# Kernel optimization log

Hardware: AMD Instinct MI355X
Metric: run time of the kernel (lower is better)

The kernel has to match this reference:

```python
import jax, jax.numpy as jnp
import numpy as np

B, S, D, H = 4, 2048, 1024, 16
HD = D // H
DFF = 4 * D
NUM_LAYERS = 12
RES = 1.0 / float(np.sqrt(NUM_LAYERS))
SCALE = 1.0 / float(np.sqrt(D))  # module divides by sqrt(embed_dim), not head_dim
EPS = 1e-5


def setup_inputs() -> dict:
    key = jax.random.key(0)
    ks = jax.random.split(key, 12)
    s = 0.02
    p = lambda k, shp: (jax.random.normal(k, shp, jnp.float32) * s)
    return {
        "x": jax.random.normal(ks[0], (B, S, D), jnp.float32),
        "Wq": p(ks[1], (D, D)), "bq": jnp.zeros((D,), jnp.float32),
        "Wk": p(ks[2], (D, D)), "bk": jnp.zeros((D,), jnp.float32),
        "Wv": p(ks[3], (D, D)), "bv": jnp.zeros((D,), jnp.float32),
        "Wo": p(ks[4], (D, D)), "bo": jnp.zeros((D,), jnp.float32),
        "g1": jnp.ones((D,), jnp.float32), "be1": jnp.zeros((D,), jnp.float32),
        "g2": jnp.ones((D,), jnp.float32), "be2": jnp.zeros((D,), jnp.float32),
        "W1": p(ks[5], (D, DFF)), "b1": jnp.zeros((DFF,), jnp.float32),
        "W2": p(ks[6], (DFF, D)), "b2": jnp.zeros((D,), jnp.float32),
    }


def _layernorm(x, g, b):
    m = jnp.mean(x, axis=-1, keepdims=True)
    v = jnp.mean((x - m) ** 2, axis=-1, keepdims=True)
    return (x - m) * jax.lax.rsqrt(v + EPS) * g + b


def _attention(x, Wq, bq, Wk, bk, Wv, bv, Wo, bo):
    b, s, d = x.shape
    q = (x @ Wq + bq).reshape(b, s, H, HD)
    k = (x @ Wk + bk).reshape(b, s, H, HD)
    v = (x @ Wv + bv).reshape(b, s, H, HD)
    scores = jnp.einsum('bqhd,bkhd->bhqk', q, k) * SCALE  # [B,H,S,S]
    mask = jnp.tril(jnp.ones((s, s), dtype=bool))
    scores = jnp.where(mask, scores, -jnp.inf)
    attn = jax.nn.softmax(scores, axis=-1)  # dropout_rate=0 -> identity
    out = jnp.einsum('bhqk,bkhd->bqhd', attn, v).reshape(b, s, d)
    return out @ Wo + bo


def reference(x, Wq, bq, Wk, bk, Wv, bv, Wo, bo, g1, be1, g2, be2, W1, b1, W2, b2):
    x = x + RES * _attention(_layernorm(x, g1, be1), Wq, bq, Wk, bk, Wv, bv, Wo, bo)
    h = _layernorm(x, g2, be2)
    ffn = jax.nn.relu(h @ W1 + b1) @ W2 + b2
    x = x + RES * ffn
    return x
```

## Files before the change

kernel.cpp:

```cpp
#include <hip/hip_runtime.h>

typedef unsigned short ushort_t;
typedef unsigned int uint32;
typedef __attribute__((ext_vector_type(4))) float f32x4;
typedef __attribute__((ext_vector_type(8))) short bf16x8;

#define B_   4
#define S_   2048
#define D_   1024
#define H_   16
#define HD_  64
#define DFF_ 4096
#define M_   (B_ * S_)

#define RES_   0.28867513459481287f
#define SCALE_ 0.03125f
#define EPS_   1e-5f
#define LOG2E_ 1.4426950408889634f

__device__ __forceinline__ ushort_t f2bf(float f) {
    union { float f; uint32 u; } c; c.f = f;
    uint32 u = c.u + 0x7fffu + ((c.u >> 16) & 1u);
    return (ushort_t)(u >> 16);
}
__device__ __forceinline__ float bf2f(ushort_t h) {
    union { uint32 u; float f; } c; c.u = ((uint32)h) << 16;
    return c.f;
}
__device__ __forceinline__ float fexp2(float x) {
    float r; asm("v_exp_f32 %0, %1" : "=v"(r) : "v"(x)); return r;
}
__device__ __forceinline__ uint32 cvt_pk_bf16(float lo, float hi) {
    uint32 r;
    asm("v_cvt_pk_bf16_f32 %0, %1, %2" : "=v"(r) : "v"(lo), "v"(hi));
    return r;
}

__global__ __launch_bounds__(256) void transpose_cast_kernel(
    const float* __restrict__ W, ushort_t* __restrict__ Wt, int K, int N)
{
    __shared__ float tile[32][33];
    const int bx = blockIdx.x * 32;
    const int by = blockIdx.y * 32;
    const int tx = threadIdx.x;
    const int ty = threadIdx.y;
    #pragma unroll
    for (int i = 0; i < 32; i += 8)
        tile[ty + i][tx] = W[(size_t)(by + ty + i) * N + bx + tx];
    __syncthreads();
    #pragma unroll
    for (int i = 0; i < 32; i += 8)
        Wt[(size_t)(bx + ty + i) * K + by + tx] = f2bf(tile[tx][ty + i]);
}

__global__ void concat_bias_kernel(const float* __restrict__ bq,
                                   const float* __restrict__ bk,
                                   const float* __restrict__ bv,
                                   float* __restrict__ bqkv)
{
    int i = blockIdx.x * blockDim.x + threadIdx.x;
    if (i < 3 * D_) {
        float v = (i < D_) ? bq[i] : (i < 2 * D_) ? bk[i - D_] : bv[i - 2 * D_];
        bqkv[i] = v;
    }
}

__global__ __launch_bounds__(256) void ln_kernel(
    const float* __restrict__ x, const float* __restrict__ g,
    const float* __restrict__ be, ushort_t* __restrict__ out)
{
    const int row = blockIdx.x;
    const int t = threadIdx.x;
    const int lane = t & 63;
    const int wave = t >> 6;
    const float4* xr = (const float4*)(x + (size_t)row * D_);
    float4 v = xr[t];
    float s  = v.x + v.y + v.z + v.w;
    float s2 = v.x * v.x + v.y * v.y + v.z * v.z + v.w * v.w;
    #pragma unroll
    for (int off = 32; off; off >>= 1) {
        s  += __shfl_xor(s, off);
        s2 += __shfl_xor(s2, off);
    }
    __shared__ float red[8];
    if (lane == 0) { red[wave * 2] = s; red[wave * 2 + 1] = s2; }
    __syncthreads();
    s  = red[0] + red[2] + red[4] + red[6];
    s2 = red[1] + red[3] + red[5] + red[7];
    const float mean = s * (1.0f / D_);
    const float var  = s2 * (1.0f / D_) - mean * mean;
    const float rstd = rsqrtf(var + EPS_);
    const float4 gv  = ((const float4*)g)[t];
    const float4 bv  = ((const float4*)be)[t];
    ushort_t o[4];
    o[0] = f2bf((v.x - mean) * rstd * gv.x + bv.x);
    o[1] = f2bf((v.y - mean) * rstd * gv.y + bv.y);
    o[2] = f2bf((v.z - mean) * rstd * gv.z + bv.z);
    o[3] = f2bf((v.w - mean) * rstd * gv.w + bv.w);
    *(ushort2*)&out[(size_t)row * D_ + t * 4]     = make_ushort2(o[0], o[1]);
    *(ushort2*)&out[(size_t)row * D_ + t * 4 + 2] = make_ushort2(o[2], o[3]);
}

template <int MODE, int BM>
__global__ __launch_bounds__((BM == 256) ? 512 : 256, (BM == 256) ? 2 : 3)
void gemm_bt3_kernel(
    const ushort_t* __restrict__ A, const ushort_t* __restrict__ Bt,
    const float* __restrict__ bias, const float* __restrict__ res,
    void* __restrict__ Cout, int M, int N, int K, int gx)
{
    constexpr int THREADS = (BM == 256) ? 512 : 256;
    constexpr int APASS = (BM * 4) / THREADS;
    constexpr int BPASS = (128 * 4) / THREADS;
    constexpr int LOADS = APASS + BPASS;

    __shared__ __align__(16) ushort_t As[3][BM * 32];
    __shared__ __align__(16) ushort_t Bs[3][128 * 32];

    const int tid  = threadIdx.x;
    const int w    = tid >> 6;
    const int lane = tid & 63;
    const int l15  = lane & 15;
    const int g    = lane >> 4;

    const int cpx = gridDim.x >> 3;
    const int swz = (blockIdx.x & 7) * cpx + (blockIdx.x >> 3);
    const int bx = swz % gx, by = swz / gx;
    const int m0 = by * BM, n0 = bx * 128;

    const int wm = (w >> 1) * 64;
    const int wn = (w & 1) * 64;

    const ushort_t* srcA[APASS];
    const ushort_t* srcB[BPASS];
    int ldsA[APASS], ldsB[BPASS];
    #pragma unroll
    for (int p = 0; p < APASS; ++p) {
        const int L = p * THREADS + tid;
        srcA[p] = A + (size_t)(m0 + (L >> 2)) * K + (L & 3) * 8;
        ldsA[p] = (p * THREADS + w * 64) * 8;
    }
    #pragma unroll
    for (int p = 0; p < BPASS; ++p) {
        const int L = p * THREADS + tid;
        srcB[p] = Bt + (size_t)(n0 + (L >> 2)) * K + (L & 3) * 8;
        ldsB[p] = (p * THREADS + w * 64) * 8;
    }

    #define STAGE(t_, buf_)                                                        \
        do {                                                                       \
            _Pragma("unroll")                                                      \
            for (int p = 0; p < APASS; ++p)                                        \
                __builtin_amdgcn_global_load_lds(                                  \
                    (const __attribute__((address_space(1))) void*)(srcA[p] + (t_) * 32), \
                    (__attribute__((address_space(3))) void*)(&As[buf_][ldsA[p]]), 16, 0, 0); \
            _Pragma("unroll")                                                      \
            for (int p = 0; p < BPASS; ++p)                                        \
                __builtin_amdgcn_global_load_lds(                                  \
                    (const __attribute__((address_space(1))) void*)(srcB[p] + (t_) * 32), \
                    (__attribute__((address_space(3))) void*)(&Bs[buf_][ldsB[p]]), 16, 0, 0); \
        } while (0)

    f32x4 acc[4][4] = {};
    const int NT = K >> 5;

    STAGE(0, 0);
    STAGE(1, 1);
    asm volatile("s_waitcnt vmcnt(%0)" :: "n"(LOADS) : "memory");
    __builtin_amdgcn_s_barrier();

    for (int t = 0; t < NT; ++t) {
        const int cur = t % 3;
        const bool more = (t + 2 < NT);
        if (more) STAGE(t + 2, (t + 2) % 3);

        bf16x8 af[4], bfr[4];
        #pragma unroll
        for (int mf = 0; mf < 4; ++mf)
            af[mf] = *(const bf16x8*)&As[cur][(wm + mf * 16 + l15) * 32 + g * 8];
        #pragma unroll
        for (int nf = 0; nf < 4; ++nf)
            bfr[nf] = *(const bf16x8*)&Bs[cur][(wn + nf * 16 + l15) * 32 + g * 8];

        __builtin_amdgcn_s_setprio(1);
        #pragma unroll
        for (int mf = 0; mf < 4; ++mf)
            #pragma unroll
            for (int nf = 0; nf < 4; ++nf)
                acc[mf][nf] = __builtin_amdgcn_mfma_f32_16x16x32_bf16(
                    af[mf], bfr[nf], acc[mf][nf], 0, 0, 0);
        __builtin_amdgcn_s_setprio(0);

        if (more)
            asm volatile("s_waitcnt vmcnt(%0)" :: "n"(LOADS) : "memory");
        else
            asm volatile("s_waitcnt vmcnt(0)" ::: "memory");
        __builtin_amdgcn_s_barrier();
    }
    #undef STAGE

    const int rbase = g * 4;
    #pragma unroll
    for (int mf = 0; mf < 4; ++mf) {
        #pragma unroll
        for (int nf = 0; nf < 4; ++nf) {
            const int col = n0 + wn + nf * 16 + l15;
            const float bcol = bias[col];
            #pragma unroll
            for (int r = 0; r < 4; ++r) {
                const int row = m0 + wm + mf * 16 + rbase + r;
                float v = acc[mf][nf][r] + bcol;
                const size_t idx = (size_t)row * N + col;
                if (MODE == 0) {
                    ((ushort_t*)Cout)[idx] = f2bf(v);
                } else if (MODE == 1) {
                    ((ushort_t*)Cout)[idx] = f2bf(fmaxf(v, 0.0f));
                } else {
                    ((float*)Cout)[idx] = res[idx] + RES_ * v;
                }
            }
        }
    }
}

__global__ __launch_bounds__(256) void fattn_kernel(
    const ushort_t* __restrict__ qkv, ushort_t* __restrict__ out)
{
    __shared__ __align__(16) ushort_t Ks[64 * 64];
    __shared__ __align__(16) ushort_t Vt[64 * 64];
    __shared__ __align__(16) ushort_t Ps[4][16 * 64];

    const int tid  = threadIdx.x;
    const int lane = tid & 63;
    const int w    = tid >> 6;
    const int bh = blockIdx.y;
    const int b = bh >> 4, h = bh & 15;

    const int l15 = lane & 15;
    const int g   = lane >> 4;

    const size_t rs = 3 * D_;
    const ushort_t* Qg = qkv + (size_t)b * S_ * rs + h * HD_;
    const ushort_t* Kg = Qg + D_;

    const int skey = tid >> 3;
    const int sc   = tid & 7;

    #pragma unroll
    for (int half = 0; half < 2; ++half) {
        const int qt = half ? blockIdx.x : (S_ / 64 - 1) - blockIdx.x;
        const int q0 = qt * 64;
        const int nkb = qt + 1;

        bf16x8 qf[2];
        {
            const int qrow = q0 + w * 16 + l15;
            #pragma unroll
            for (int kk = 0; kk < 2; ++kk) {
                bf16x8 tq = *(const bf16x8*)(Qg + (size_t)qrow * rs + kk * 32 + g * 8);
                #pragma unroll
                for (int e = 0; e < 8; ++e)
                    tq[e] = (short)f2bf(bf2f((ushort_t)tq[e]) * (SCALE_ * LOG2E_));
                qf[kk] = tq;
            }
        }

        float mrow = -1e30f, lrow = 0.f;
        f32x4 oacc[4] = {};

        bf16x8 kvreg[2], vvreg[2];
        #pragma unroll
        for (int pass = 0; pass < 2; ++pass) {
            const ushort_t* src = Kg + (size_t)(pass * 32 + skey) * rs + sc * 8;
            kvreg[pass] = *(const bf16x8*)src;
            vvreg[pass] = *(const bf16x8*)(src + D_);
        }

        for (int kb = 0; kb < nkb; ++kb) {
            __syncthreads();
            #pragma unroll
            for (int pass = 0; pass < 2; ++pass) {
                const int key = pass * 32 + skey;
                *(bf16x8*)&Ks[key * 64 + ((sc ^ (key & 7)) << 3)] = kvreg[pass];
                #pragma unroll
                for (int j = 0; j < 8; ++j) {
                    const int d  = sc * 8 + j;
                    const int cp = (key >> 3) ^ (d & 7) ^ ((d >> 3) & 7);
                    Vt[d * 64 + (cp << 3) + (key & 7)] = (ushort_t)vvreg[pass][j];
                }
            }
            if (kb + 1 < nkb) {
                #pragma unroll
                for (int pass = 0; pass < 2; ++pass) {
                    const ushort_t* src =
                        Kg + (size_t)((kb + 1) * 64 + pass * 32 + skey) * rs + sc * 8;
                    kvreg[pass] = *(const bf16x8*)src;
                    vvreg[pass] = *(const bf16x8*)(src + D_);
                }
            }
            __syncthreads();

            f32x4 sf[4] = {};
            __builtin_amdgcn_s_setprio(1);
            #pragma unroll
            for (int kk = 0; kk < 2; ++kk) {
                const int cc = kk * 4 + g;
                #pragma unroll
                for (int nf = 0; nf < 4; ++nf) {
                    const int keyr = nf * 16 + l15;
                    bf16x8 kf = *(const bf16x8*)&Ks[keyr * 64 + ((cc ^ (keyr & 7)) << 3)];
                    sf[nf] = __builtin_amdgcn_mfma_f32_16x16x32_bf16(kf, qf[kk], sf[nf], 0, 0, 0);
                }
            }
            __builtin_amdgcn_s_setprio(0);

            if (kb == nkb - 1) {
                const int q = q0 + w * 16 + l15;
                #pragma unroll
                for (int nf = 0; nf < 4; ++nf)
                    #pragma unroll
                    for (int r = 0; r < 4; ++r)
                        if (kb * 64 + nf * 16 + g * 4 + r > q) sf[nf][r] = -1e30f;
            }
            float mx = -1e30f;
            #pragma unroll
            for (int nf = 0; nf < 4; ++nf)
                #pragma unroll
                for (int r = 0; r < 4; ++r) mx = fmaxf(mx, sf[nf][r]);
            mx = fmaxf(mx, __shfl_xor(mx, 16));
            mx = fmaxf(mx, __shfl_xor(mx, 32));

            if (!__all(mx - mrow <= 8.0f)) {
                const float mnew = fmaxf(mrow, mx);
                const float corr = fexp2(mrow - mnew);
                mrow = mnew;
                lrow *= corr;
                #pragma unroll
                for (int r = 0; r < 4; ++r) {
                    const float cr = __shfl(corr, g * 4 + r, 16);
                    #pragma unroll
                    for (int nf = 0; nf < 4; ++nf) oacc[nf][r] *= cr;
                }
            }

            {
                const int qrow = l15;
                float psum = 0.f;
                #pragma unroll
                for (int nf = 0; nf < 4; ++nf) {
                    const float p0 = fexp2(sf[nf][0] - mrow);
                    const float p1 = fexp2(sf[nf][1] - mrow);
                    const float p2 = fexp2(sf[nf][2] - mrow);
                    const float p3 = fexp2(sf[nf][3] - mrow);
                    psum += (p0 + p1) + (p2 + p3);
                    uint2 pk = make_uint2(cvt_pk_bf16(p0, p1), cvt_pk_bf16(p2, p3));
                    const int c16 = ((nf << 1) + (g >> 1)) ^ (qrow & 7);
                    *(uint2*)((char*)Ps[w] + qrow * 128 + c16 * 16 + (g & 1) * 8) = pk;
                }
                psum += __shfl_xor(psum, 16);
                psum += __shfl_xor(psum, 32);
                lrow += psum;
            }

            #pragma unroll
            for (int kk = 0; kk < 2; ++kk) {
                const int cc = kk * 4 + g;
                const int qrow = l15;
                const int c16 = cc ^ (qrow & 7);
                bf16x8 pa = *(const bf16x8*)((const char*)Ps[w] + qrow * 128 + c16 * 16);
                __builtin_amdgcn_s_setprio(1);
                #pragma unroll
                for (int nf = 0; nf < 4; ++nf) {
                    const int dr  = nf * 16 + l15;
                    const int cvp = cc ^ (dr & 7) ^ ((dr >> 3) & 7);
                    bf16x8 vf = *(const bf16x8*)&Vt[dr * 64 + (cvp << 3)];
                    oacc[nf] = __builtin_amdgcn_mfma_f32_16x16x32_bf16(pa, vf, oacc[nf], 0, 0, 0);
                }
                __builtin_amdgcn_s_setprio(0);
            }
        }

        const float linv = 1.0f / lrow;
        #pragma unroll
        for (int r = 0; r < 4; ++r) {
            const float li = __shfl(linv, g * 4 + r, 16);
            const int q = q0 + w * 16 + g * 4 + r;
            ushort_t* op = out + (size_t)(b * S_ + q) * D_ + h * HD_;
            #pragma unroll
            for (int nf = 0; nf < 4; ++nf)
                op[nf * 16 + l15] = f2bf(oacc[nf][r] * li);
        }
    }
}

extern "C" void kernel_launch(void* const* d_in, const int* in_sizes, int n_in,
                              void* d_out, int out_size, void* d_ws, size_t ws_size,
                              hipStream_t stream)
{
    const float* x   = (const float*)d_in[0];
    const float* Wq  = (const float*)d_in[1];
    const float* bq  = (const float*)d_in[2];
    const float* Wk  = (const float*)d_in[3];
    const float* bk  = (const float*)d_in[4];
    const float* Wv  = (const float*)d_in[5];
    const float* bv  = (const float*)d_in[6];
    const float* Wo  = (const float*)d_in[7];
    const float* bo  = (const float*)d_in[8];
    const float* g1  = (const float*)d_in[9];
    const float* be1 = (const float*)d_in[10];
    const float* g2  = (const float*)d_in[11];
    const float* be2 = (const float*)d_in[12];
    const float* W1  = (const float*)d_in[13];
    const float* b1  = (const float*)d_in[14];
    const float* W2  = (const float*)d_in[15];
    const float* b2  = (const float*)d_in[16];
    float* out = (float*)d_out;

    char* ws = (char*)d_ws;
    size_t o = 0;
    auto alloc = [&](size_t bytes) { size_t r = o; o = (o + bytes + 255) & ~(size_t)255; return r; };
    ushort_t* Wqkvt = (ushort_t*)(ws + alloc((size_t)3 * D_ * D_ * 2));
    ushort_t* Wot   = (ushort_t*)(ws + alloc((size_t)D_ * D_ * 2));
    ushort_t* W1t   = (ushort_t*)(ws + alloc((size_t)DFF_ * D_ * 2));
    ushort_t* W2t   = (ushort_t*)(ws + alloc((size_t)D_ * DFF_ * 2));
    float*    bqkv  = (float*)(ws + alloc((size_t)3 * D_ * 4));
    ushort_t* lnbuf = (ushort_t*)(ws + alloc((size_t)M_ * D_ * 2));
    ushort_t* bigbuf= (ushort_t*)(ws + alloc((size_t)M_ * DFF_ * 2));
    ushort_t* attnb = (ushort_t*)(ws + alloc((size_t)M_ * D_ * 2));
    float*    x1    = (float*)(ws + alloc((size_t)M_ * D_ * 4));

    dim3 tblock(32, 8);
    transpose_cast_kernel<<<dim3(D_/32, D_/32), tblock, 0, stream>>>(Wq, Wqkvt,            D_, D_);
    transpose_cast_kernel<<<dim3(D_/32, D_/32), tblock, 0, stream>>>(Wk, Wqkvt + D_*D_,    D_, D_);
    transpose_cast_kernel<<<dim3(D_/32, D_/32), tblock, 0, stream>>>(Wv, Wqkvt + 2*D_*D_,  D_, D_);
    transpose_cast_kernel<<<dim3(D_/32, D_/32), tblock, 0, stream>>>(Wo, Wot,              D_, D_);
    transpose_cast_kernel<<<dim3(DFF_/32, D_/32), tblock, 0, stream>>>(W1, W1t,            D_, DFF_);
    transpose_cast_kernel<<<dim3(D_/32, DFF_/32), tblock, 0, stream>>>(W2, W2t,            DFF_, D_);
    concat_bias_kernel<<<12, 256, 0, stream>>>(bq, bk, bv, bqkv);

    ln_kernel<<<M_, 256, 0, stream>>>(x, g1, be1, lnbuf);
    gemm_bt3_kernel<0, 256><<<(M_/256)*(3*D_/128), 512, 0, stream>>>(
        lnbuf, Wqkvt, bqkv, nullptr, bigbuf, M_, 3*D_, D_, 3*D_/128);
    fattn_kernel<<<dim3(S_/128, B_*H_), 256, 0, stream>>>(bigbuf, attnb);
    gemm_bt3_kernel<2, 128><<<(M_/128)*(D_/128), 256, 0, stream>>>(
        attnb, Wot, bo, x, x1, M_, D_, D_, D_/128);
    ln_kernel<<<M_, 256, 0, stream>>>(x1, g2, be2, lnbuf);
    gemm_bt3_kernel<1, 256><<<(M_/256)*(DFF_/128), 512, 0, stream>>>(
        lnbuf, W1t, b1, nullptr, bigbuf, M_, DFF_, D_, DFF_/128);
    gemm_bt3_kernel<2, 128><<<(M_/128)*(D_/128), 256, 0, stream>>>(
        bigbuf, W2t, b2, x1, out, M_, D_, DFF_, D_/128);
}
```

Before: 410.7 us.

## Switch GEMMs to 32x32x16 MFMA with XOR-swizzled LDS and uniform 128x128 tiles

Rewrites the GEMM kernel to use 32x32x16 bf16 MFMA instructions with a 2x2 accumulator grid per wave instead of 4x4 16x16x32 tiles. An XOR swizzle on the 16-byte chunk index is applied on the global-to-LDS load side and undone on the LDS reads, to cut bank conflicts. The BM=256/512-thread variant is dropped, so the QKV and FFN1 GEMMs now use the same 128x128 tile with 256 threads. The larger MFMA shape reduces LDS fragment traffic per flop, but the smaller tiles on the big GEMMs lower data reuse and raise the block count.

New measurement: 481.9 us. +17.3%, slower.

```diff
diff --git a/kernel.cpp b/kernel.cpp
--- a/kernel.cpp
+++ b/kernel.cpp
@@ -3,6 +3,7 @@
 typedef unsigned short ushort_t;
 typedef unsigned int uint32;
 typedef __attribute__((ext_vector_type(4))) float f32x4;
+typedef __attribute__((ext_vector_type(16))) float f32x16;
 typedef __attribute__((ext_vector_type(8))) short bf16x8;
 
 #define B_   4
@@ -35,6 +36,11 @@
     asm("v_cvt_pk_bf16_f32 %0, %1, %2" : "=v"(r) : "v"(lo), "v"(hi));
     return r;
 }
+
+#define GLDS(src_, dst_)                                                     \
+    __builtin_amdgcn_global_load_lds(                                        \
+        (const __attribute__((address_space(1))) void*)(src_),               \
+        (__attribute__((address_space(3))) void*)(dst_), 16, 0, 0)
 
 __global__ __launch_bounds__(256) void transpose_cast_kernel(
     const float* __restrict__ W, ushort_t* __restrict__ Wt, int K, int N)
@@ -101,71 +107,62 @@
     *(ushort2*)&out[(size_t)row * D_ + t * 4 + 2] = make_ushort2(o[2], o[3]);
 }
 
-template <int MODE, int BM>
-__global__ __launch_bounds__((BM == 256) ? 512 : 256, (BM == 256) ? 2 : 3)
-void gemm_bt3_kernel(
+template <int MODE>
+__global__ __launch_bounds__(256, 3) void gemm32_kernel(
     const ushort_t* __restrict__ A, const ushort_t* __restrict__ Bt,
     const float* __restrict__ bias, const float* __restrict__ res,
     void* __restrict__ Cout, int M, int N, int K, int gx)
 {
-    constexpr int THREADS = (BM == 256) ? 512 : 256;
-    constexpr int APASS = (BM * 4) / THREADS;
-    constexpr int BPASS = (128 * 4) / THREADS;
-    constexpr int LOADS = APASS + BPASS;
-
-    __shared__ __align__(16) ushort_t As[3][BM * 32];
+    __shared__ __align__(16) ushort_t As[3][128 * 32];
     __shared__ __align__(16) ushort_t Bs[3][128 * 32];
 
     const int tid  = threadIdx.x;
     const int w    = tid >> 6;
     const int lane = tid & 63;
-    const int l15  = lane & 15;
-    const int g    = lane >> 4;
+    const int l31  = lane & 31;
+    const int g2   = lane >> 5;
+    const int rp   = l31 & 3;
 
     const int cpx = gridDim.x >> 3;
     const int swz = (blockIdx.x & 7) * cpx + (blockIdx.x >> 3);
     const int bx = swz % gx, by = swz / gx;
-    const int m0 = by * BM, n0 = bx * 128;
+    const int m0 = by * 128, n0 = bx * 128;
 
     const int wm = (w >> 1) * 64;
     const int wn = (w & 1) * 64;
 
-    const ushort_t* srcA[APASS];
-    const ushort_t* srcB[BPASS];
-    int ldsA[APASS], ldsB[BPASS];
-    #pragma unroll
-    for (int p = 0; p < APASS; ++p) {
-        const int L = p * THREADS + tid;
-        srcA[p] = A + (size_t)(m0 + (L >> 2)) * K + (L & 3) * 8;
-        ldsA[p] = (p * THREADS + w * 64) * 8;
-    }
-    #pragma unroll
-    for (int p = 0; p < BPASS; ++p) {
-        const int L = p * THREADS + tid;
-        srcB[p] = Bt + (size_t)(n0 + (L >> 2)) * K + (L & 3) * 8;
-        ldsB[p] = (p * THREADS + w * 64) * 8;
-    }
-
-    #define STAGE(t_, buf_)                                                        \
-        do {                                                                       \
-            _Pragma("unroll")                                                      \
-            for (int p = 0; p < APASS; ++p)                                        \
-                __builtin_amdgcn_global_load_lds(                                  \
-                    (const __attribute__((address_space(1))) void*)(srcA[p] + (t_) * 32), \
-                    (__attribute__((address_space(3))) void*)(&As[buf_][ldsA[p]]), 16, 0, 0); \
-            _Pragma("unroll")                                                      \
-            for (int p = 0; p < BPASS; ++p)                                        \
-                __builtin_amdgcn_global_load_lds(                                  \
-                    (const __attribute__((address_space(1))) void*)(srcB[p] + (t_) * 32), \
-                    (__attribute__((address_space(3))) void*)(&Bs[buf_][ldsB[p]]), 16, 0, 0); \
+    const ushort_t* srcA[2];
+    const ushort_t* srcB[2];
+    int ldsA[2], ldsB[2];
+    #pragma unroll
+    for (int p = 0; p < 2; ++p) {
+        const int L = p * 256 + tid;
+        const int row = L >> 2;
+        srcA[p] = A  + (size_t)(m0 + row) * K + (((L & 3) ^ (row & 3)) << 3);
+        srcB[p] = Bt + (size_t)(n0 + row) * K + (((L & 3) ^ (row & 3)) << 3);
+        ldsA[p] = (p * 256 + w * 64) * 8;
+        ldsB[p] = (p * 256 + w * 64) * 8;
+    }
+
+    #define STAGE(t_, buf_)                                                  \
+        do {                                                                 \
+            GLDS(srcA[0] + (size_t)(t_) * 32, &As[buf_][ldsA[0]]);           \
+            GLDS(srcA[1] + (size_t)(t_) * 32, &As[buf_][ldsA[1]]);           \
+            GLDS(srcB[0] + (size_t)(t_) * 32, &Bs[buf_][ldsB[0]]);           \
+            GLDS(srcB[1] + (size_t)(t_) * 32, &Bs[buf_][ldsB[1]]);           \
         } while (0)
 
-    f32x4 acc[4][4] = {};
+    #define LDA(mf_, kk_) (*(const bf16x8*)&As[cur][(wm + (mf_) * 32 + l31) * 32 + \
+                              ((((kk_) * 2 + g2) ^ rp) << 3)])
+    #define LDB(nf_, kk_) (*(const bf16x8*)&Bs[cur][(wn + (nf_) * 32 + l31) * 32 + \
+                              ((((kk_) * 2 + g2) ^ rp) << 3)])
+
+    f32x16 acc[2][2] = {};
     const int NT = K >> 5;
 
     STAGE(0, 0);
     STAGE(1, 1);
-    asm volatile("s_waitcnt vmcnt(%0)" :: "n"(LOADS) : "memory");
+    asm volatile("s_waitcnt vmcnt(4)" ::: "memory");
     __builtin_amdgcn_s_barrier();
 
     for (int t = 0; t < NT; ++t) {
@@ -173,41 +170,41 @@
         const bool more = (t + 2 < NT);
         if (more) STAGE(t + 2, (t + 2) % 3);
 
-        bf16x8 af[4], bfr[4];
-        #pragma unroll
-        for (int mf = 0; mf < 4; ++mf)
-            af[mf] = *(const bf16x8*)&As[cur][(wm + mf * 16 + l15) * 32 + g * 8];
-        #pragma unroll
-        for (int nf = 0; nf < 4; ++nf)
-            bfr[nf] = *(const bf16x8*)&Bs[cur][(wn + nf * 16 + l15) * 32 + g * 8];
+        bf16x8 a0k0 = LDA(0, 0), a1k0 = LDA(1, 0);
+        bf16x8 b0k0 = LDB(0, 0), b1k0 = LDB(1, 0);
+        bf16x8 a0k1 = LDA(0, 1), a1k1 = LDA(1, 1);
+        bf16x8 b0k1 = LDB(0, 1), b1k1 = LDB(1, 1);
 
         __builtin_amdgcn_s_setprio(1);
-        #pragma unroll
-        for (int mf = 0; mf < 4; ++mf)
-            #pragma unroll
-            for (int nf = 0; nf < 4; ++nf)
-                acc[mf][nf] = __builtin_amdgcn_mfma_f32_16x16x32_bf16(
-                    af[mf], bfr[nf], acc[mf][nf], 0, 0, 0);
+        acc[0][0] = __builtin_amdgcn_mfma_f32_32x32x16_bf16(a0k0, b0k0, acc[0][0], 0, 0, 0);
+        acc[0][1] = __builtin_amdgcn_mfma_f32_32x32x16_bf16(a0k0, b1k0, acc[0][1], 0, 0, 0);
+        acc[1][0] = __builtin_amdgcn_mfma_f32_32x32x16_bf16(a1k0, b0k0, acc[1][0], 0, 0, 0);
+        acc[1][1] = __builtin_amdgcn_mfma_f32_32x32x16_bf16(a1k0, b1k0, acc[1][1], 0, 0, 0);
+        acc[0][0] = __builtin_amdgcn_mfma_f32_32x32x16_bf16(a0k1, b0k1, acc[0][0], 0, 0, 0);
+        acc[0][1] = __builtin_amdgcn_mfma_f32_32x32x16_bf16(a0k1, b1k1, acc[0][1], 0, 0, 0);
+        acc[1][0] = __builtin_amdgcn_mfma_f32_32x32x16_bf16(a1k1, b0k1, acc[1][0], 0, 0, 0);
+        acc[1][1] = __builtin_amdgcn_mfma_f32_32x32x16_bf16(a1k1, b1k1, acc[1][1], 0, 0, 0);
         __builtin_amdgcn_s_setprio(0);
 
         if (more)
-            asm volatile("s_waitcnt vmcnt(%0)" :: "n"(LOADS) : "memory");
+            asm volatile("s_waitcnt vmcnt(4)" ::: "memory");
         else
             asm volatile("s_waitcnt vmcnt(0)" ::: "memory");
         __builtin_amdgcn_s_barrier();
     }
     #undef STAGE
-
-    const int rbase = g * 4;
-    #pragma unroll
-    for (int mf = 0; mf < 4; ++mf) {
+    #undef LDA
+    #undef LDB
+
+    #pragma unroll
+    for (int mf = 0; mf < 2; ++mf) {
         #pragma unroll
-        for (int nf = 0; nf < 4; ++nf) {
-            const int col = n0 + wn + nf * 16 + l15;
+        for (int nf = 0; nf < 2; ++nf) {
+            const int col = n0 + wn + nf * 32 + l31;
             const float bcol = bias[col];
             #pragma unroll
-            for (int r = 0; r < 4; ++r) {
-                const int row = m0 + wm + mf * 16 + rbase + r;
+            for (int r = 0; r < 16; ++r) {
+                const int row = m0 + wm + mf * 32 + (r & 3) + 8 * (r >> 2) + 4 * g2;
                 float v = acc[mf][nf][r] + bcol;
                 const size_t idx = (size_t)row * N + col;
                 if (MODE == 0) {
@@ -438,14 +435,14 @@
     concat_bias_kernel<<<12, 256, 0, stream>>>(bq, bk, bv, bqkv);
 
     ln_kernel<<<M_, 256, 0, stream>>>(x, g1, be1, lnbuf);
-    gemm_bt3_kernel<0, 256><<<(M_/256)*(3*D_/128), 512, 0, stream>>>(
+    gemm32_kernel<0><<<(M_/128)*(3*D_/128), 256, 0, stream>>>(
         lnbuf, Wqkvt, bqkv, nullptr, bigbuf, M_, 3*D_, D_, 3*D_/128);
     fattn_kernel<<<dim3(S_/128, B_*H_), 256, 0, stream>>>(bigbuf, attnb);
-    gemm_bt3_kernel<2, 128><<<(M_/128)*(D_/128), 256, 0, stream>>>(
+    gemm32_kernel<2><<<(M_/128)*(D_/128), 256, 0, stream>>>(
         attnb, Wot, bo, x, x1, M_, D_, D_, D_/128);
     ln_kernel<<<M_, 256, 0, stream>>>(x1, g2, be2, lnbuf);
-    gemm_bt3_kernel<1, 256><<<(M_/256)*(DFF_/128), 512, 0, stream>>>(
+    gemm32_kernel<1><<<(M_/128)*(DFF_/128), 256, 0, stream>>>(
         lnbuf, W1t, b1, nullptr, bigbuf, M_, DFF_, D_, DFF_/128);
-    gemm_bt3_kernel<2, 128><<<(M_/128)*(D_/128), 256, 0, stream>>>(
+    gemm32_kernel<2><<<(M_/128)*(D_/128), 256, 0, stream>>>(
         bigbuf, W2t, b2, x1, out, M_, D_, DFF_, D_/128);
 }
```
